# Optimization experiments

Hardware: AMD Instinct MI355X
Metric: run time of the kernel (lower is better)

The kernel has to match this reference:

```python
import jax, jax.numpy as jnp
import numpy as np

B, D_IN, D_H, N_ACT, N_HEADS = 64, 512, 512, 16, 8
EPS = 1e-6


def setup_inputs() -> dict:
    key = jax.random.key(0)
    ks = jax.random.split(key, 4)
    s = lambda fan_in: 1.0 / np.sqrt(fan_in).astype(np.float32)
    return {
        "x": jax.random.normal(ks[0], (B, D_IN), jnp.float32),
        "Wh": jax.random.normal(ks[1], (D_IN, D_H), jnp.float32) * s(D_IN),
        "bh": jnp.zeros((D_H,), jnp.float32),
        "ln_scale": jnp.ones((D_H,), jnp.float32),
        "ln_bias": jnp.zeros((D_H,), jnp.float32),
        "Wz1": jax.random.normal(ks[2], (D_IN + N_ACT, N_HEADS * D_H), jnp.float32) * s(D_IN + N_ACT),
        "Wz2": jax.random.normal(ks[3], (D_IN + N_ACT, N_HEADS * D_H), jnp.float32) * s(D_IN + N_ACT),
    }


def reference(x, Wh, bh, ln_scale, ln_bias, Wz1, Wz2):
    # h = LayerNorm(relu(fc_h(x)))
    h_pre = jax.nn.relu(x @ Wh + bh)                      # (B, D_H)
    mu = jnp.mean(h_pre, axis=-1, keepdims=True)
    var = jnp.var(h_pre, axis=-1, keepdims=True)
    h = (h_pre - mu) / jnp.sqrt(var + EPS) * ln_scale + ln_bias

    # input conditioning: repeat x per action, concat one-hot action
    x_rep = jnp.repeat(x, N_ACT, axis=0)                  # (B*A, D_IN)
    onehot = jnp.tile(jnp.eye(N_ACT, dtype=jnp.float32), (x.shape[0], 1))
    xc = jnp.concatenate([x_rep, onehot], axis=-1)        # (B*A, D_IN+A)

    z1 = (xc @ Wz1).reshape(-1, N_HEADS, D_H)             # (B*A, H, D_H)
    z2 = (xc @ Wz2).reshape(-1, N_HEADS, D_H)             # (B*A, H, D_G=D_H)

    # bilinear scores over tiny contraction dim H, then row norm + tanh
    w = jnp.einsum('bhg,bhd->bgd', z2, z1)                # (B*A, D_G, D_H)
    w = (w - jnp.mean(w, axis=-1, keepdims=True)) / (jnp.std(w, axis=-1, keepdims=True) + EPS)
    w = jnp.tanh(w)

    v = jnp.repeat(h, N_ACT, axis=0)                      # (B*A, D_H)
    y_ = jnp.einsum('bgd,bd->bg', w, v)                   # (B*A, D_G)

    # goodness 'msq'
    logits = jnp.mean(jnp.square(y_), axis=1)[:, None]    # (B*A, 1)
    q = logits.reshape(-1, N_ACT)                         # (B, A)
    return h, q, y_
```

## Files before the change

kernel.cpp:

```cpp
#include <hip/hip_runtime.h>
#include <math.h>

#define EPS 1e-6f

typedef _Float16 half8 __attribute__((ext_vector_type(8)));
typedef _Float16 half2v __attribute__((ext_vector_type(2)));
typedef __fp16  fp16x2r __attribute__((ext_vector_type(2)));
typedef float f32x16 __attribute__((ext_vector_type(16)));

__device__ __forceinline__ half2v cvt_pk(float a, float b) {
    fp16x2r v = __builtin_amdgcn_cvt_pkrtz(a, b);
    return __builtin_bit_cast(half2v, v);
}

__device__ __forceinline__ float fdot2f(half2v a, half2v b, float c) {
#if __has_builtin(__builtin_amdgcn_fdot2)
    return __builtin_amdgcn_fdot2(__builtin_bit_cast(fp16x2r, a),
                                  __builtin_bit_cast(fp16x2r, b), c, false);
#else
    return fmaf((float)a[0], (float)b[0], fmaf((float)a[1], (float)b[1], c));
#endif
}

__global__ __launch_bounds__(256) void k_xh(
    const float* __restrict__ x, _Float16* __restrict__ xh,
    float* __restrict__ zbuf) {
    const int tid = blockIdx.x * 256 + threadIdx.x;
    const int i = tid * 8;
    float4 a = *(const float4*)(x + i);
    float4 b = *(const float4*)(x + i + 4);
    half8 o;
    o[0] = (_Float16)a.x; o[1] = (_Float16)a.y; o[2] = (_Float16)a.z; o[3] = (_Float16)a.w;
    o[4] = (_Float16)b.x; o[5] = (_Float16)b.y; o[6] = (_Float16)b.z; o[7] = (_Float16)b.w;
    *(half8*)(xh + i) = o;

    const float4 z = {0.f, 0.f, 0.f, 0.f};
#pragma unroll 2
    for (int j = tid * 4; j < 557056; j += 4096 * 4)
        *(float4*)(zbuf + j) = z;
}

__global__ __launch_bounds__(256) void k_gemm(
    const _Float16* __restrict__ xh, const float* __restrict__ Wh,
    const float* __restrict__ Wz1, const float* __restrict__ Wz2,
    float* __restrict__ hpre, float* __restrict__ xz1,
    float* __restrict__ xz2) {
    const int s  = blockIdx.x;
    const int k0 = blockIdx.y * 256;
    const int t  = threadIdx.x;
    const int l  = t & 63, w = t >> 6;
    const int hi = l >> 5, l31 = l & 31;
    const int cbase = s * 128;

    const float* __restrict__ W;
    float* __restrict__ out;
    int ncols, ocol;
    if (s < 4)       { W = Wh;  out = hpre; ncols = 512;  ocol = cbase; }
    else if (s < 36) { W = Wz1; out = xz1;  ncols = 4096; ocol = cbase - 512; }
    else             { W = Wz2; out = xz2;  ncols = 4096; ocol = cbase - 4608; }

    const int col = ocol + 32 * w + l31;

    const f32x16 CZ = {0.f, 0.f, 0.f, 0.f, 0.f, 0.f, 0.f, 0.f,
                       0.f, 0.f, 0.f, 0.f, 0.f, 0.f, 0.f, 0.f};
    f32x16 acc0 = CZ;
    f32x16 acc1 = CZ;

    const _Float16* __restrict__ a0p = xh + l31 * 512 + 8 * hi + k0;
    const _Float16* __restrict__ a1p = a0p + 32 * 512;
    const float* __restrict__    wp  = W + (size_t)(k0 + 8 * hi) * ncols + col;

#pragma unroll 2
    for (int kk = 0; kk < 256; kk += 16) {
        half8 a0 = *(const half8*)(a0p + kk);
        half8 a1 = *(const half8*)(a1p + kk);
        const float* wk = wp + (size_t)kk * ncols;
        half8 bf;
#pragma unroll
        for (int j = 0; j < 8; ++j)
            bf[j] = (_Float16)wk[(size_t)j * ncols];
        acc0 = __builtin_amdgcn_mfma_f32_32x32x16_f16(a0, bf, acc0, 0, 0, 0);
        acc1 = __builtin_amdgcn_mfma_f32_32x32x16_f16(a1, bf, acc1, 0, 0, 0);
    }
#pragma unroll
    for (int i = 0; i < 16; ++i) {
        const int m = (i & 3) + 8 * (i >> 2) + 4 * hi;
        atomicAdd(out + (size_t)m * ncols + col,        acc0[i]);
        atomicAdd(out + (size_t)(m + 32) * ncols + col, acc1[i]);
    }
}

__global__ __launch_bounds__(256) void k_mid(
    const float* __restrict__ hpre, const float* __restrict__ bh,
    const float* __restrict__ ls, const float* __restrict__ lb,
    const float* __restrict__ xz1, const float* __restrict__ xz2,
    const float* __restrict__ Wz1, const float* __restrict__ Wz2,
    float* __restrict__ hout,
    _Float16* __restrict__ z1h, _Float16* __restrict__ z2h,
    _Float16* __restrict__ z2bh, float* __restrict__ qout) {
    const int t  = threadIdx.x;
    const int l  = t & 63, wv = t >> 6;

    __shared__ float red[44 * 4];
    __shared__ float Ssum[44];

    if (blockIdx.x < 64) {
        const int b = blockIdx.x;
        if (t < 16) qout[b * 16 + t] = 0.f;
        float h0 = fmaxf(hpre[b * 512 + t]       + bh[t],       0.f);
        float h1 = fmaxf(hpre[b * 512 + t + 256] + bh[t + 256], 0.f);
        float s = h0 + h1, ss = h0 * h0 + h1 * h1;
#pragma unroll
        for (int m = 1; m < 64; m <<= 1) {
            s  += __shfl_xor(s, m);
            ss += __shfl_xor(ss, m);
        }
        if (l == 0) { red[wv] = s; red[4 + wv] = ss; }
        __syncthreads();
        s  = red[0] + red[1] + red[2] + red[3];
        ss = red[4] + red[5] + red[6] + red[7];
        float mean = s * (1.0f / 512.0f);
        float var  = ss * (1.0f / 512.0f) - mean * mean;
        float rstd = rsqrtf(var + EPS);
        hout[b * 512 + t]       = (h0 - mean) * rstd * ls[t]       + lb[t];
        hout[b * 512 + t + 256] = (h1 - mean) * rstd * ls[t + 256] + lb[t + 256];
        return;
    }

    const int r  = blockIdx.x - 64;
    const int br = r >> 4, a = r & 15;

    const float* __restrict__ x1  = xz1 + br * 4096;
    const float* __restrict__ x2  = xz2 + br * 4096;
    const float* __restrict__ w1r = Wz1 + (512 + a) * 4096;
    const float* __restrict__ w2r = Wz2 + (512 + a) * 4096;

    float pm[8], pg[36];
#pragma unroll
    for (int i = 0; i < 8; ++i) pm[i] = 0.f;
#pragma unroll
    for (int i = 0; i < 36; ++i) pg[i] = 0.f;

    half8 h2keep[2];
#pragma unroll
    for (int p = 0; p < 2; ++p) {
        const int d = t + p * 256;
        half8 h1, h2;
#pragma unroll
        for (int h = 0; h < 8; ++h) {
            float z1v = x1[h * 512 + d] + w1r[h * 512 + d];
            float z2v = x2[h * 512 + d] + w2r[h * 512 + d];
            h1[h] = (_Float16)z1v;
            h2[h] = (_Float16)z2v;
        }
        *(half8*)(z1h + ((size_t)r * 512 + d) * 8) = h1;
        h2keep[p] = h2;
        float zr[8];
#pragma unroll
        for (int h = 0; h < 8; ++h) zr[h] = (float)h1[h];
#pragma unroll
        for (int h = 0; h < 8; ++h) pm[h] += zr[h];
        int id = 0;
#pragma unroll
        for (int h = 0; h < 8; ++h)
#pragma unroll
            for (int h2_ = h; h2_ < 8; ++h2_) { pg[id] += zr[h] * zr[h2_]; ++id; }
    }

#pragma unroll
    for (int m = 1; m < 64; m <<= 1) {
#pragma unroll
        for (int i = 0; i < 8; ++i)  pm[i] += __shfl_xor(pm[i], m);
#pragma unroll
        for (int i = 0; i < 36; ++i) pg[i] += __shfl_xor(pg[i], m);
    }
    if (l == 0) {
#pragma unroll
        for (int i = 0; i < 8; ++i)  red[i * 4 + wv]       = pm[i];
#pragma unroll
        for (int i = 0; i < 36; ++i) red[(8 + i) * 4 + wv] = pg[i];
    }
    __syncthreads();
    if (t < 44) Ssum[t] = red[t * 4 + 0] + red[t * 4 + 1] + red[t * 4 + 2] + red[t * 4 + 3];
    __syncthreads();

#pragma unroll
    for (int p = 0; p < 2; ++p) {
        const int g = t + p * 256;
        float zv[8];
#pragma unroll
        for (int h = 0; h < 8; ++h) zv[h] = (float)h2keep[p][h];
        float mean = 0.f;
#pragma unroll
        for (int h = 0; h < 8; ++h) mean = fmaf(zv[h], Ssum[h], mean);
        mean *= (1.0f / 512.0f);
        float e2 = 0.f;
        int id = 0;
#pragma unroll
        for (int h = 0; h < 8; ++h)
#pragma unroll
            for (int h2_ = h; h2_ < 8; ++h2_) {
                float p2 = zv[h] * zv[h2_] * Ssum[8 + id];
                e2 += (h2_ == h) ? p2 : 2.0f * p2;
                ++id;
            }
        e2 *= (1.0f / 512.0f);
        float var  = e2 - mean * mean;
        float sd   = sqrtf(fmaxf(var, 0.f));
        float rstd = 1.0f / (sd + EPS);
        z2bh[r * 512 + g] = (_Float16)(-mean * rstd);
        half8 hs;
#pragma unroll
        for (int h = 0; h < 8; ++h) hs[h] = (_Float16)(zv[h] * rstd);
        *(half8*)(z2h + ((size_t)r * 512 + g) * 8) = hs;
    }
}

__global__ __launch_bounds__(256, 6) void k_main(
    const _Float16* __restrict__ z1h, const _Float16* __restrict__ z2h,
    const _Float16* __restrict__ z2bh, const float* __restrict__ hbuf,
    float* __restrict__ yout, float* __restrict__ qout) {
    const int bx = blockIdx.x;
    const int r  = bx >> 1, gh = bx & 1;
    const int br = r >> 4;
    const int t  = threadIdx.x;
    const int l  = t & 63, wv = t >> 6;
    const int hi = l >> 5, l31 = l & 31;

    __shared__ __align__(16) _Float16 z1t[513 * 8];
    __shared__ half2v vs2[256];
    __shared__ float ys[256];
    __shared__ float wq[4];

#pragma unroll
    for (int p = 0; p < 2; ++p) {
        const int d = t + p * 256;
        *(half8*)(z1t + d * 8) = *(const half8*)(z1h + ((size_t)r * 512 + d) * 8);
    }
    if (t == 0) {
        half8 one = {};
        one[0] = (_Float16)1.0f;
        *(half8*)(z1t + 512 * 8) = one;
    }

    {
        const float* __restrict__ vrow = hbuf + br * 512;
        const int np_ = t >> 5, j_ = t & 31;
        vs2[t] = cvt_pk(vrow[np_ * 64 + j_], vrow[np_ * 64 + 32 + j_]);
    }
    __syncthreads();

    const half2v CLO = {(_Float16)-2.5f, (_Float16)-2.5f};
    const half2v CHI = {(_Float16) 2.5f, (_Float16) 2.5f};
    const half2v C0  = {(_Float16)0.98335470f, (_Float16)0.98335470f};
    const half2v C1  = {(_Float16)-0.24780080f, (_Float16)-0.24780080f};
    const half2v C2  = {(_Float16)0.04040730f, (_Float16)0.04040730f};
    const half2v C3  = {(_Float16)-0.00252110f, (_Float16)-0.00252110f};

    const f32x16 CZ = {0.f, 0.f, 0.f, 0.f, 0.f, 0.f, 0.f, 0.f,
                       0.f, 0.f, 0.f, 0.f, 0.f, 0.f, 0.f, 0.f};
    float qacc = 0.f;
#pragma unroll 1
    for (int mi = 0; mi < 2; ++mi) {
        const int m0 = (wv * 2 + mi) * 32;
        half8 Af;
        if (hi) {
            half8 tmp = {};
            tmp[0] = z2bh[(size_t)r * 512 + gh * 256 + m0 + l31];
            Af = tmp;
        } else {
            Af = *(const half8*)(z2h + ((size_t)r * 512 + gh * 256 + m0 + l31) * 8);
        }
        float yac[16];
#pragma unroll
        for (int i = 0; i < 16; ++i) yac[i] = 0.f;

#pragma unroll 1
        for (int np = 0; np < 8; ++np) {
            const int n0 = np * 64;
            const int browa = hi ? 512 : (n0 + l31);
            const int browb = hi ? 512 : (n0 + 32 + l31);
            const half8 Ba = *(const half8*)(z1t + browa * 8);
            const half8 Bb = *(const half8*)(z1t + browb * 8);
            f32x16 Da = __builtin_amdgcn_mfma_f32_32x32x16_f16(Af, Ba, CZ, 0, 0, 0);
            f32x16 Db = __builtin_amdgcn_mfma_f32_32x32x16_f16(Af, Bb, CZ, 0, 0, 0);
            const half2v vv = vs2[np * 32 + l31];
#pragma unroll
            for (int i = 0; i < 16; ++i) {
                half2v tt = cvt_pk(Da[i], Db[i]);
                tt = __builtin_elementwise_max(tt, CLO);
                tt = __builtin_elementwise_min(tt, CHI);
                half2v u  = tt * tt;
                half2v pp = C3 * u + C2;
                pp = pp * u + C1;
                pp = pp * u + C0;
                half2v wt = tt * pp;
                yac[i] = fdot2f(wt, vv, yac[i]);
            }
        }
#pragma unroll
        for (int i = 0; i < 16; ++i) {
#pragma unroll
            for (int m = 1; m <= 16; m <<= 1) yac[i] += __shfl_xor(yac[i], m);
        }
        if (l31 == 0) {
#pragma unroll
            for (int i = 0; i < 16; ++i) {
                const int g = m0 + (i & 3) + 8 * (i >> 2) + 4 * hi;
                float yv = yac[i];
                ys[g] = yv;
                qacc = fmaf(yv, yv, qacc);
            }
        }
    }
    qacc += __shfl_xor(qacc, 32);
    if (l == 0) wq[wv] = qacc;
    __syncthreads();
    if (t == 0) atomicAdd(qout + r, (wq[0] + wq[1] + wq[2] + wq[3]) * (1.0f / 512.0f));
    yout[r * 512 + gh * 256 + t] = ys[t];
}

extern "C" void kernel_launch(void* const* d_in, const int* in_sizes, int n_in,
                              void* d_out, int out_size, void* d_ws, size_t ws_size,
                              hipStream_t stream) {
    const float* x   = (const float*)d_in[0];
    const float* Wh  = (const float*)d_in[1];
    const float* bh  = (const float*)d_in[2];
    const float* ls  = (const float*)d_in[3];
    const float* lb  = (const float*)d_in[4];
    const float* Wz1 = (const float*)d_in[5];
    const float* Wz2 = (const float*)d_in[6];

    float* out  = (float*)d_out;
    float* hout = out;
    float* qout = out + 32768;
    float* yout = out + 33792;

    char* ws = (char*)d_ws;
    float*     xz1  = (float*)(ws);
    float*     xz2  = (float*)(ws + (1u << 20));
    float*     hpre = (float*)(ws + (2u << 20));
    _Float16*  xh   = (_Float16*)(ws + (2u << 20) + 135168);
    _Float16*  z2bh = (_Float16*)(ws + (2u << 20) + 200704);
    _Float16*  z1h  = (_Float16*)(ws + (4u << 20));
    _Float16*  z2h  = z1h + (size_t)1024 * 512 * 8;

    k_xh  <<<16, 256, 0, stream>>>(x, xh, (float*)ws);
    k_gemm<<<dim3(68, 2), 256, 0, stream>>>(xh, Wh, Wz1, Wz2, hpre, xz1, xz2);
    k_mid <<<1088, 256, 0, stream>>>(hpre, bh, ls, lb, xz1, xz2, Wz1, Wz2,
                                     hout, z1h, z2h, z2bh, qout);
    k_main<<<2048, 256, 0, stream>>>(z1h, z2h, z2bh, hout, yout, qout);
}
```

Baseline: 87.09 us.

## Swap MFMA operand roles so reduction over d stays in-lane, one block per row

k_main now puts z1 (the d dimension) on the MFMA A side and z2 (g) on B, so each lane accumulates y for a fixed g directly across the 16 accumulator entries. This replaces the 80-shuffle cross-lane reduction with a single shuffle per output. v is prepacked in LDS to match the accumulator layout. One block now covers a whole row (1024 blocks instead of 2048), which removes the atomic on q and the q zeroing in k_mid. Each wave keeps four B fragments in registers, raising register pressure, and launch bounds drop to 4 waves per SIMD.

```diff
diff --git a/kernel.cpp b/kernel.cpp
--- a/kernel.cpp
+++ b/kernel.cpp
@@ -20,6 +20,30 @@
 #else
     return fmaf((float)a[0], (float)b[0], fmaf((float)a[1], (float)b[1], c));
 #endif
+}
+
+__device__ __forceinline__ float tile_finish(const f32x16& D, uint4 va, uint4 vb,
+                                             float yg) {
+    const half2v CLO = {(_Float16)-2.5f, (_Float16)-2.5f};
+    const half2v CHI = {(_Float16) 2.5f, (_Float16) 2.5f};
+    const half2v C0  = {(_Float16)0.98335470f, (_Float16)0.98335470f};
+    const half2v C1  = {(_Float16)-0.24780080f, (_Float16)-0.24780080f};
+    const half2v C2  = {(_Float16)0.04040730f, (_Float16)0.04040730f};
+    const half2v C3  = {(_Float16)-0.00252110f, (_Float16)-0.00252110f};
+#define PAIR(jj, word) {                                          \
+        half2v tt = cvt_pk(D[2*jj], D[2*jj+1]);                   \
+        tt = __builtin_elementwise_max(tt, CLO);                  \
+        tt = __builtin_elementwise_min(tt, CHI);                  \
+        half2v u  = tt * tt;                                      \
+        half2v pp = C3 * u + C2;                                  \
+        pp = pp * u + C1;                                         \
+        pp = pp * u + C0;                                         \
+        half2v wt = tt * pp;                                      \
+        yg = fdot2f(wt, __builtin_bit_cast(half2v, word), yg); }
+    PAIR(0, va.x) PAIR(1, va.y) PAIR(2, va.z) PAIR(3, va.w)
+    PAIR(4, vb.x) PAIR(5, vb.y) PAIR(6, vb.z) PAIR(7, vb.w)
+#undef PAIR
+    return yg;
 }
 
 __global__ __launch_bounds__(256) void k_xh(
@@ -97,7 +121,7 @@
     const float* __restrict__ Wz1, const float* __restrict__ Wz2,
     float* __restrict__ hout,
     _Float16* __restrict__ z1h, _Float16* __restrict__ z2h,
-    _Float16* __restrict__ z2bh, float* __restrict__ qout) {
+    _Float16* __restrict__ z2bh) {
     const int t  = threadIdx.x;
     const int l  = t & 63, wv = t >> 6;
 
@@ -106,7 +130,6 @@
 
     if (blockIdx.x < 64) {
         const int b = blockIdx.x;
-        if (t < 16) qout[b * 16 + t] = 0.f;
         float h0 = fmaxf(hpre[b * 512 + t]       + bh[t],       0.f);
         float h1 = fmaxf(hpre[b * 512 + t + 256] + bh[t + 256], 0.f);
         float s = h0 + h1, ss = h0 * h0 + h1 * h1;
@@ -216,20 +239,18 @@
     }
 }
 
-__global__ __launch_bounds__(256, 6) void k_main(
+__global__ __launch_bounds__(256, 4) void k_main(
     const _Float16* __restrict__ z1h, const _Float16* __restrict__ z2h,
     const _Float16* __restrict__ z2bh, const float* __restrict__ hbuf,
     float* __restrict__ yout, float* __restrict__ qout) {
-    const int bx = blockIdx.x;
-    const int r  = bx >> 1, gh = bx & 1;
+    const int r  = blockIdx.x;
     const int br = r >> 4;
     const int t  = threadIdx.x;
     const int l  = t & 63, wv = t >> 6;
     const int hi = l >> 5, l31 = l & 31;
 
     __shared__ __align__(16) _Float16 z1t[513 * 8];
-    __shared__ half2v vs2[256];
-    __shared__ float ys[256];
+    __shared__ __align__(16) unsigned int vp[256];
     __shared__ float wq[4];
 
 #pragma unroll
@@ -242,82 +263,66 @@
         one[0] = (_Float16)1.0f;
         *(half8*)(z1t + 512 * 8) = one;
     }
-
     {
         const float* __restrict__ vrow = hbuf + br * 512;
-        const int np_ = t >> 5, j_ = t & 31;
-        vs2[t] = cvt_pk(vrow[np_ * 64 + j_], vrow[np_ * 64 + 32 + j_]);
+        const int mm = t >> 4, h2 = (t >> 3) & 1, j = t & 7;
+        const int d0 = mm * 32 + 2 * (j & 1) + 8 * (j >> 1) + 4 * h2;
+        vp[t] = __builtin_bit_cast(unsigned int, cvt_pk(vrow[d0], vrow[d0 + 1]));
     }
     __syncthreads();
 
-    const half2v CLO = {(_Float16)-2.5f, (_Float16)-2.5f};
-    const half2v CHI = {(_Float16) 2.5f, (_Float16) 2.5f};
-    const half2v C0  = {(_Float16)0.98335470f, (_Float16)0.98335470f};
-    const half2v C1  = {(_Float16)-0.24780080f, (_Float16)-0.24780080f};
-    const half2v C2  = {(_Float16)0.04040730f, (_Float16)0.04040730f};
-    const half2v C3  = {(_Float16)-0.00252110f, (_Float16)-0.00252110f};
+    const size_t gb = (size_t)r * 512 + wv * 128 + l31;
+    half8 Bf0, Bf1, Bf2, Bf3;
+    if (hi) {
+        half8 z = {};
+        Bf0 = z; Bf0[0] = z2bh[gb];
+        Bf1 = z; Bf1[0] = z2bh[gb + 32];
+        Bf2 = z; Bf2[0] = z2bh[gb + 64];
+        Bf3 = z; Bf3[0] = z2bh[gb + 96];
+    } else {
+        Bf0 = *(const half8*)(z2h + gb * 8);
+        Bf1 = *(const half8*)(z2h + (gb + 32) * 8);
+        Bf2 = *(const half8*)(z2h + (gb + 64) * 8);
+        Bf3 = *(const half8*)(z2h + (gb + 96) * 8);
+    }
 
     const f32x16 CZ = {0.f, 0.f, 0.f, 0.f, 0.f, 0.f, 0.f, 0.f,
                        0.f, 0.f, 0.f, 0.f, 0.f, 0.f, 0.f, 0.f};
-    float qacc = 0.f;
-#pragma unroll 1
-    for (int mi = 0; mi < 2; ++mi) {
-        const int m0 = (wv * 2 + mi) * 32;
-        half8 Af;
-        if (hi) {
-            half8 tmp = {};
-            tmp[0] = z2bh[(size_t)r * 512 + gh * 256 + m0 + l31];
-            Af = tmp;
-        } else {
-            Af = *(const half8*)(z2h + ((size_t)r * 512 + gh * 256 + m0 + l31) * 8);
-        }
-        float yac[16];
-#pragma unroll
-        for (int i = 0; i < 16; ++i) yac[i] = 0.f;
-
-#pragma unroll 1
-        for (int np = 0; np < 8; ++np) {
-            const int n0 = np * 64;
-            const int browa = hi ? 512 : (n0 + l31);
-            const int browb = hi ? 512 : (n0 + 32 + l31);
-            const half8 Ba = *(const half8*)(z1t + browa * 8);
-            const half8 Bb = *(const half8*)(z1t + browb * 8);
-            f32x16 Da = __builtin_amdgcn_mfma_f32_32x32x16_f16(Af, Ba, CZ, 0, 0, 0);
-            f32x16 Db = __builtin_amdgcn_mfma_f32_32x32x16_f16(Af, Bb, CZ, 0, 0, 0);
-            const half2v vv = vs2[np * 32 + l31];
-#pragma unroll
-            for (int i = 0; i < 16; ++i) {
-                half2v tt = cvt_pk(Da[i], Db[i]);
-                tt = __builtin_elementwise_max(tt, CLO);
-                tt = __builtin_elementwise_min(tt, CHI);
-                half2v u  = tt * tt;
-                half2v pp = C3 * u + C2;
-                pp = pp * u + C1;
-                pp = pp * u + C0;
-                half2v wt = tt * pp;
-                yac[i] = fdot2f(wt, vv, yac[i]);
-            }
-        }
-#pragma unroll
-        for (int i = 0; i < 16; ++i) {
-#pragma unroll
-            for (int m = 1; m <= 16; m <<= 1) yac[i] += __shfl_xor(yac[i], m);
-        }
-        if (l31 == 0) {
-#pragma unroll
-            for (int i = 0; i < 16; ++i) {
-                const int g = m0 + (i & 3) + 8 * (i >> 2) + 4 * hi;
-                float yv = yac[i];
-                ys[g] = yv;
-                qacc = fmaf(yv, yv, qacc);
-            }
-        }
-    }
-    qacc += __shfl_xor(qacc, 32);
+    float yg0 = 0.f, yg1 = 0.f, yg2 = 0.f, yg3 = 0.f;
+#pragma unroll 2
+    for (int m = 0; m < 16; ++m) {
+        const int arow = hi ? 512 : (m * 32 + l31);
+        const half8 Aa = *(const half8*)(z1t + arow * 8);
+        const uint4 va = *(const uint4*)(vp + (m * 2 + hi) * 8);
+        const uint4 vb = *(const uint4*)(vp + (m * 2 + hi) * 8 + 4);
+        f32x16 D0 = __builtin_amdgcn_mfma_f32_32x32x16_f16(Aa, Bf0, CZ, 0, 0, 0);
+        yg0 = tile_finish(D0, va, vb, yg0);
+        f32x16 D1 = __builtin_amdgcn_mfma_f32_32x32x16_f16(Aa, Bf1, CZ, 0, 0, 0);
+        yg1 = tile_finish(D1, va, vb, yg1);
+        f32x16 D2 = __builtin_amdgcn_mfma_f32_32x32x16_f16(Aa, Bf2, CZ, 0, 0, 0);
+        yg2 = tile_finish(D2, va, vb, yg2);
+        f32x16 D3 = __builtin_amdgcn_mfma_f32_32x32x16_f16(Aa, Bf3, CZ, 0, 0, 0);
+        yg3 = tile_finish(D3, va, vb, yg3);
+    }
+
+    yg0 += __shfl_xor(yg0, 32);
+    yg1 += __shfl_xor(yg1, 32);
+    yg2 += __shfl_xor(yg2, 32);
+    yg3 += __shfl_xor(yg3, 32);
+
+    const int gy = r * 512 + wv * 128 + l31;
+    if (!hi) {
+        yout[gy]      = yg0;
+        yout[gy + 32] = yg1;
+        yout[gy + 64] = yg2;
+        yout[gy + 96] = yg3;
+    }
+    float qacc = hi ? 0.f : (yg0 * yg0 + yg1 * yg1 + yg2 * yg2 + yg3 * yg3);
+#pragma unroll
+    for (int m = 1; m < 64; m <<= 1) qacc += __shfl_xor(qacc, m);
     if (l == 0) wq[wv] = qacc;
     __syncthreads();
-    if (t == 0) atomicAdd(qout + r, (wq[0] + wq[1] + wq[2] + wq[3]) * (1.0f / 512.0f));
-    yout[r * 512 + gh * 256 + t] = ys[t];
+    if (t == 0) qout[r] = (wq[0] + wq[1] + wq[2] + wq[3]) * (1.0f / 512.0f);
 }
 
 extern "C" void kernel_launch(void* const* d_in, const int* in_sizes, int n_in,
@@ -348,6 +353,6 @@
     k_xh  <<<16, 256, 0, stream>>>(x, xh, (float*)ws);
     k_gemm<<<dim3(68, 2), 256, 0, stream>>>(xh, Wh, Wz1, Wz2, hpre, xz1, xz2);
     k_mid <<<1088, 256, 0, stream>>>(hpre, bh, ls, lb, xz1, xz2, Wz1, Wz2,
-                                     hout, z1h, z2h, z2bh, qout);
-    k_main<<<2048, 256, 0, stream>>>(z1h, z2h, z2bh, hout, yout, qout);
-}
+                                     hout, z1h, z2h, z2bh);
+    k_main<<<1024, 256, 0, stream>>>(z1h, z2h, z2bh, hout, yout, qout);
+}
```

After: 80.36 us. 1.08x faster.
